# Kernel optimization log

Hardware: AMD Instinct MI355X
Metric: run time of the kernel (lower is better)

Reference implementation:

```python
import jax, jax.numpy as jnp
import numpy as np

B, Q, K, DQ, DK, H, DV = 4, 1024, 1024, 256, 256, 64, 256

def setup_inputs() -> dict:
    key = jax.random.key(0)
    k1, k2, k3, k4, k5, k6 = jax.random.split(key, 6)
    queries = jax.random.normal(k1, (B, Q, DQ), dtype=jnp.float32)
    keys = jax.random.normal(k2, (B, K, DK), dtype=jnp.float32)
    values = jax.random.normal(k3, (B, K, DV), dtype=jnp.float32)
    # learned params (stored as (in, out) so x @ W matches nn.Linear)
    W_q = jax.random.normal(k4, (DQ, H), dtype=jnp.float32) / np.sqrt(DQ)
    W_k = jax.random.normal(k5, (DK, H), dtype=jnp.float32) / np.sqrt(DK)
    w_v = jax.random.normal(k6, (H,), dtype=jnp.float32) / np.sqrt(H)
    return {"queries": queries, "keys": keys, "values": values,
            "W_q": W_q, "W_k": W_k, "w_v": w_v}

def reference(queries, keys, values, W_q, W_k, w_v):
    # projections: [B,Q,H], [B,K,H]
    q = jnp.einsum('bqd,dh->bqh', queries, W_q)
    k = jnp.einsum('bkd,dh->bkh', keys, W_k)
    # broadcast add -> tanh -> reduce with w_v: scores [B,Q,K]
    features = jnp.tanh(q[:, :, None, :] + k[:, None, :, :])  # [B,Q,K,H]
    scores = jnp.einsum('bqkh,h->bqk', features, w_v)
    attn = jax.nn.softmax(scores, axis=-1)  # dropout is identity in eval
    return jnp.einsum('bqk,bkv->bqv', attn, values)
```

## Files before the change

### kernel.cpp

```cpp
#include <hip/hip_runtime.h>

#define Bn 4
#define Qn 1024
#define Kn 1024
#define Dd 256
#define Hh 64
#define Dv 256
#define TQ 16

typedef __attribute__((ext_vector_type(8))) short short8;
typedef __attribute__((ext_vector_type(8))) _Float16 half8;
typedef __attribute__((ext_vector_type(4))) float floatx4;
typedef __attribute__((ext_vector_type(2))) float floatx2;

__device__ __forceinline__ floatx2 fma2(floatx2 a, floatx2 b, floatx2 c) {
    return __builtin_elementwise_fma(a, b, c);
}
__device__ __forceinline__ floatx2 mk2(float x, float y) {
    floatx2 r; r.x = x; r.y = y; return r;
}

__device__ __forceinline__ short f32_to_bf16(float x) {
    unsigned u = __float_as_uint(x);
    unsigned r = u + 0x7fffu + ((u >> 16) & 1u);
    return (short)(r >> 16);
}
__device__ __forceinline__ float bf16_to_f32(short h) {
    return __uint_as_float(((unsigned)(unsigned short)h) << 16);
}

__global__ __launch_bounds__(256) void prep_kernel(const float* __restrict__ Xq,
                                                   const float* __restrict__ Wq,
                                                   const float* __restrict__ Xk,
                                                   const float* __restrict__ Wk,
                                                   const float* __restrict__ V,
                                                   float* __restrict__ Eq,
                                                   float* __restrict__ Ekt,
                                                   _Float16* __restrict__ Vh) {
    int t = threadIdx.x;
    int wave = t >> 6, l = t & 63;
    if (blockIdx.x < 512) {
        int side = blockIdx.x >> 8;
        int r0 = (blockIdx.x & 255) * 16;
        int ct = wave;
        const float* X = side ? Xk : Xq;
        const float* W = side ? Wk : Wq;
        const float* xrow = X + (size_t)(r0 + (l & 15)) * Dd + (l >> 4) * 8;
        const float* wcol = W + (size_t)((l >> 4) * 8) * Hh + ct * 16 + (l & 15);

        floatx4 sxa[2], sxb[2];
        float swr[2][8];
#define PLOAD(kt, s) do {                                                   \
            sxa[s] = *(const floatx4*)(xrow + (kt) * 32);                   \
            sxb[s] = *(const floatx4*)(xrow + (kt) * 32 + 4);               \
            _Pragma("unroll")                                               \
            for (int j = 0; j < 8; ++j)                                     \
                swr[s][j] = wcol[(size_t)((kt) * 32 + j) * Hh];             \
        } while (0)

        PLOAD(0, 0);
        floatx4 acc = {0.f, 0.f, 0.f, 0.f};
        #pragma unroll
        for (int kt = 0; kt < 8; ++kt) {
            int cur = kt & 1;
            if (kt < 7) PLOAD(kt + 1, 1 - cur);
            short8 ah, al, wh, wl;
            #pragma unroll
            for (int j = 0; j < 4; ++j) {
                short hs = f32_to_bf16(sxa[cur][j]);
                ah[j] = hs;
                al[j] = f32_to_bf16(sxa[cur][j] - bf16_to_f32(hs));
                short hs2 = f32_to_bf16(sxb[cur][j]);
                ah[j + 4] = hs2;
                al[j + 4] = f32_to_bf16(sxb[cur][j] - bf16_to_f32(hs2));
            }
            #pragma unroll
            for (int j = 0; j < 8; ++j) {
                short hs = f32_to_bf16(swr[cur][j]);
                wh[j] = hs;
                wl[j] = f32_to_bf16(swr[cur][j] - bf16_to_f32(hs));
            }
            acc = __builtin_amdgcn_mfma_f32_16x16x32_bf16(ah, wh, acc, 0, 0, 0);
            acc = __builtin_amdgcn_mfma_f32_16x16x32_bf16(al, wh, acc, 0, 0, 0);
            acc = __builtin_amdgcn_mfma_f32_16x16x32_bf16(ah, wl, acc, 0, 0, 0);
        }
#undef PLOAD
        int h = ct * 16 + (l & 15);
        float e0 = __expf(2.f * acc[0]);
        float e1 = __expf(2.f * acc[1]);
        float e2 = __expf(2.f * acc[2]);
        float e3 = __expf(2.f * acc[3]);
        int row0g = r0 + (l >> 4) * 4;
        if (!side) {
            Eq[(size_t)(row0g + 0) * Hh + h] = e0;
            Eq[(size_t)(row0g + 1) * Hh + h] = e1;
            Eq[(size_t)(row0g + 2) * Hh + h] = e2;
            Eq[(size_t)(row0g + 3) * Hh + h] = e3;
        } else {
            int b = row0g >> 10, k0 = row0g & 1023;
            float4 o = { e0, e1, e2, e3 };
            *(float4*)(Ekt + ((size_t)(b * Hh + h)) * Kn + k0) = o;
        }
    } else {
        int vblk = blockIdx.x - 512;
        int b = vblk >> 5;
        int kt = vblk & 31;
        const float* Vg = V + ((size_t)(b * Kn + kt * 32 + (l >> 4) * 8)) * Dv + (l & 15);
        #pragma unroll
        for (int p = 0; p < 4; ++p) {
            int nt = wave * 4 + p;
            const float* vp = Vg + nt * 16;
            half8 hv;
            #pragma unroll
            for (int j = 0; j < 8; ++j)
                hv[j] = (_Float16)vp[(size_t)j * Dv];
            size_t base = (((size_t)(b * 32 + kt) * 16 + nt) * 512) + (size_t)l * 8;
            *(half8*)(Vh + base) = hv;
        }
    }
}

__global__ __launch_bounds__(1024, 4) void attn_kernel(const float* __restrict__ Eq,
                                                       const float* __restrict__ Ekt,
                                                       const _Float16* __restrict__ Vh,
                                                       const float* __restrict__ wv,
                                                       float* __restrict__ out) {
    __shared__ __align__(16) unsigned sc[TQ * 1028];
    __shared__ __align__(16) float qlds[TQ * Hh];
    __shared__ float wsum[16 * TQ];

    int tid = threadIdx.x;
    int blk = blockIdx.x;
    int b = (blk & 7) >> 1;
    int tile = (blk >> 3) * 2 + (blk & 1);
    int qbase = tile * TQ;

    const float* qp = Eq + (size_t)(b * Qn + qbase) * Hh;
    qlds[tid] = qp[tid];
    __syncthreads();

    const float* kb = Ekt + (size_t)b * Hh * Kn;
    const float4* wv4 = (const float4*)wv;
    floatx2 s2[TQ / 2];
    #pragma unroll
    for (int i = 0; i < TQ / 2; ++i) { s2[i].x = 0.f; s2[i].y = 0.f; }

    float e0 = kb[0 * Kn + tid];
    float e1 = kb[1 * Kn + tid];
    float e2 = kb[2 * Kn + tid];
    float e3 = kb[3 * Kn + tid];
    floatx2 one2 = mk2(1.f, 1.f);
    for (int h4 = 0; h4 < Hh / 4; ++h4) {
        float n0, n1, n2, n3;
        if (h4 < Hh / 4 - 1) {
            const float* kn = kb + (h4 + 1) * 4 * Kn;
            n0 = kn[0 * Kn + tid];
            n1 = kn[1 * Kn + tid];
            n2 = kn[2 * Kn + tid];
            n3 = kn[3 * Kn + tid];
        }
        float4 w4 = wv4[h4];
        floatx2 e0s = mk2(e0, e0), e1s = mk2(e1, e1);
        floatx2 e2s = mk2(e2, e2), e3s = mk2(e3, e3);
        floatx2 wx = mk2(w4.x, w4.x), wy = mk2(w4.y, w4.y);
        floatx2 wz = mk2(w4.z, w4.z), ww = mk2(w4.w, w4.w);
        #pragma unroll
        for (int qq = 0; qq < TQ; qq += 2) {
            float4 qva = *(const float4*)(&qlds[qq * Hh + h4 * 4]);
            float4 qvb = *(const float4*)(&qlds[(qq + 1) * Hh + h4 * 4]);
            floatx2 A = fma2(mk2(qva.x, qvb.x), e0s, one2);
            floatx2 B = fma2(mk2(qva.y, qvb.y), e1s, one2);
            floatx2 C = fma2(mk2(qva.z, qvb.z), e2s, one2);
            floatx2 D = fma2(mk2(qva.w, qvb.w), e3s, one2);
            floatx2 AB = A * B;
            floatx2 CD = C * D;
            floatx2 ABCD = AB * CD;
            floatx2 NAB = fma2(wx, B, wy * A);
            floatx2 NCD = fma2(wz, D, ww * C);
            floatx2 NUM = fma2(NCD, AB, NAB * CD);
            floatx2 R = mk2(__builtin_amdgcn_rcpf(ABCD.x),
                            __builtin_amdgcn_rcpf(ABCD.y));
            s2[qq >> 1] = fma2(NUM, R, s2[qq >> 1]);
        }
        e0 = n0; e1 = n1; e2 = n2; e3 = n3;
    }

    int wave = tid >> 6, lane = tid & 63;
    size_t vb0 = (((size_t)(b * 32) * 16 + wave) * 512) + (size_t)lane * 8;
    half8 vcur = *(const half8*)(Vh + vb0);

    _Float16* sp = (_Float16*)sc;
    float part[TQ];
    #pragma unroll
    for (int q = 0; q < TQ; ++q) {
        float sq = (q & 1) ? s2[q >> 1].y : s2[q >> 1].x;
        float p = __expf(-2.f * sq);
        part[q] = p;
        _Float16 hs = (_Float16)p;
        sp[q * 2056 + tid] = hs;
        sp[q * 2056 + 1024 + tid] = (_Float16)(p - (float)hs);
    }

    #pragma unroll
    for (int q = 0; q < TQ; ++q) {
        #pragma unroll
        for (int off = 32; off >= 1; off >>= 1)
            part[q] += __shfl_xor(part[q], off, 64);
    }
    if (lane == 0) {
        #pragma unroll
        for (int q = 0; q < TQ; ++q) wsum[wave * TQ + q] = part[q];
    }
    __syncthreads();

    int qf = lane & 15, kc = lane >> 4;
    floatx4 acc = {0.f, 0.f, 0.f, 0.f};
    const char* scb = (const char*)sc + qf * 4112 + kc * 16;
    #pragma unroll 2
    for (int kt = 0; kt < 31; ++kt) {
        half8 vnext = *(const half8*)(Vh + vb0 + (size_t)(kt + 1) * 8192);
        half8 bhi = *(const half8*)(scb + kt * 64);
        half8 blo = *(const half8*)(scb + 2048 + kt * 64);
        acc = __builtin_amdgcn_mfma_f32_16x16x32_f16(vcur, bhi, acc, 0, 0, 0);
        acc = __builtin_amdgcn_mfma_f32_16x16x32_f16(vcur, blo, acc, 0, 0, 0);
        vcur = vnext;
    }
    {
        half8 bhi = *(const half8*)(scb + 31 * 64);
        half8 blo = *(const half8*)(scb + 2048 + 31 * 64);
        acc = __builtin_amdgcn_mfma_f32_16x16x32_f16(vcur, bhi, acc, 0, 0, 0);
        acc = __builtin_amdgcn_mfma_f32_16x16x32_f16(vcur, blo, acc, 0, 0, 0);
    }
    {
        float vsum = 0.f;
        #pragma unroll
        for (int w = 0; w < 16; ++w) vsum += wsum[w * TQ + qf];
        float r = 1.f / vsum;
        float* ob = out + ((size_t)(b * Qn + qbase + qf)) * Dv + wave * 16 + kc * 4;
        float4 o = { acc[0] * r, acc[1] * r, acc[2] * r, acc[3] * r };
        *(float4*)ob = o;
    }
}

extern "C" void kernel_launch(void* const* d_in, const int* in_sizes, int n_in,
                              void* d_out, int out_size, void* d_ws, size_t ws_size,
                              hipStream_t stream) {
    const float* queries = (const float*)d_in[0];
    const float* keys    = (const float*)d_in[1];
    const float* values  = (const float*)d_in[2];
    const float* W_q     = (const float*)d_in[3];
    const float* W_k     = (const float*)d_in[4];
    const float* w_v     = (const float*)d_in[5];
    float* out = (float*)d_out;

    float* Eq  = (float*)d_ws;
    float* Ekt = Eq + Bn * Qn * Hh;
    _Float16* Vh = (_Float16*)(Ekt + Bn * Kn * Hh);

    prep_kernel<<<640, 256, 0, stream>>>(queries, W_q, keys, W_k, values,
                                         Eq, Ekt, Vh);
    attn_kernel<<<Bn * (Qn / TQ), 1024, 0, stream>>>(Eq, Ekt, Vh, w_v, out);
}
```

Measured before the change: 115.2 us.

## Fuse prep and attention into one cooperative kernel with grid sync

Merges the projection/exp prep kernel and the attention kernel into a single cooperative launch of 256 blocks. Ten waves per block do the prep jobs, then a grid-wide barrier and scalar cache invalidate separate that phase from attention. Eq is now stored transposed, so the attention phase reads q values directly from global memory as 16-wide vectors instead of staging them in LDS. This removes one kernel launch and the gap between kernels, at the cost of a grid sync, less parallelism during the prep phase, and redundant global q loads in every thread.

```diff
diff --git a/kernel.cpp b/kernel.cpp
--- a/kernel.cpp
+++ b/kernel.cpp
@@ -1,4 +1,7 @@
 #include <hip/hip_runtime.h>
+#include <hip/hip_cooperative_groups.h>
+
+namespace cg = cooperative_groups;
 
 #define Bn 4
 #define Qn 1024
@@ -12,6 +15,7 @@
 typedef __attribute__((ext_vector_type(8))) _Float16 half8;
 typedef __attribute__((ext_vector_type(4))) float floatx4;
 typedef __attribute__((ext_vector_type(2))) float floatx2;
+typedef __attribute__((ext_vector_type(16))) float floatx16;
 
 __device__ __forceinline__ floatx2 fma2(floatx2 a, floatx2 b, floatx2 c) {
     return __builtin_elementwise_fma(a, b, c);
@@ -29,105 +33,103 @@
     return __uint_as_float(((unsigned)(unsigned short)h) << 16);
 }
 
-__global__ __launch_bounds__(256) void prep_kernel(const float* __restrict__ Xq,
-                                                   const float* __restrict__ Wq,
-                                                   const float* __restrict__ Xk,
-                                                   const float* __restrict__ Wk,
-                                                   const float* __restrict__ V,
-                                                   float* __restrict__ Eq,
-                                                   float* __restrict__ Ekt,
-                                                   _Float16* __restrict__ Vh) {
-    int t = threadIdx.x;
-    int wave = t >> 6, l = t & 63;
-    if (blockIdx.x < 512) {
-        int side = blockIdx.x >> 8;
-        int r0 = (blockIdx.x & 255) * 16;
-        int ct = wave;
-        const float* X = side ? Xk : Xq;
-        const float* W = side ? Wk : Wq;
-        const float* xrow = X + (size_t)(r0 + (l & 15)) * Dd + (l >> 4) * 8;
-        const float* wcol = W + (size_t)((l >> 4) * 8) * Hh + ct * 16 + (l & 15);
-
-        floatx4 sxa[2], sxb[2];
-        float swr[2][8];
+__global__ __launch_bounds__(1024) void fused_kernel(const float* __restrict__ Xq,
+                                                     const float* __restrict__ Wq,
+                                                     const float* __restrict__ Xk,
+                                                     const float* __restrict__ Wk,
+                                                     const float* __restrict__ V,
+                                                     const float* __restrict__ wv,
+                                                     float* __restrict__ Eqt,
+                                                     float* __restrict__ Ekt,
+                                                     _Float16* __restrict__ Vh,
+                                                     float* __restrict__ out) {
+    __shared__ __align__(16) unsigned sc[TQ * 1028];
+    __shared__ float wsum[16 * TQ];
+
+    {
+        int wave = threadIdx.x >> 6, l = threadIdx.x & 63;
+        int job = blockIdx.x * 10 + wave;
+        if (wave < 10) {
+            if (job < 2048) {
+                int bo = job >> 2;
+                int side = bo >> 8;
+                int r0 = (bo & 255) * 16;
+                int ct = job & 3;
+                const float* X = side ? Xk : Xq;
+                const float* W = side ? Wk : Wq;
+                const float* xrow = X + (size_t)(r0 + (l & 15)) * Dd + (l >> 4) * 8;
+                const float* wcol = W + (size_t)((l >> 4) * 8) * Hh + ct * 16 + (l & 15);
+
+                floatx4 sxa[2], sxb[2];
+                float swr[2][8];
 #define PLOAD(kt, s) do {                                                   \
-            sxa[s] = *(const floatx4*)(xrow + (kt) * 32);                   \
-            sxb[s] = *(const floatx4*)(xrow + (kt) * 32 + 4);               \
-            _Pragma("unroll")                                               \
-            for (int j = 0; j < 8; ++j)                                     \
-                swr[s][j] = wcol[(size_t)((kt) * 32 + j) * Hh];             \
-        } while (0)
-
-        PLOAD(0, 0);
-        floatx4 acc = {0.f, 0.f, 0.f, 0.f};
-        #pragma unroll
-        for (int kt = 0; kt < 8; ++kt) {
-            int cur = kt & 1;
-            if (kt < 7) PLOAD(kt + 1, 1 - cur);
-            short8 ah, al, wh, wl;
-            #pragma unroll
-            for (int j = 0; j < 4; ++j) {
-                short hs = f32_to_bf16(sxa[cur][j]);
-                ah[j] = hs;
-                al[j] = f32_to_bf16(sxa[cur][j] - bf16_to_f32(hs));
-                short hs2 = f32_to_bf16(sxb[cur][j]);
-                ah[j + 4] = hs2;
-                al[j + 4] = f32_to_bf16(sxb[cur][j] - bf16_to_f32(hs2));
+                    sxa[s] = *(const floatx4*)(xrow + (kt) * 32);           \
+                    sxb[s] = *(const floatx4*)(xrow + (kt) * 32 + 4);       \
+                    _Pragma("unroll")                                       \
+                    for (int j = 0; j < 8; ++j)                             \
+                        swr[s][j] = wcol[(size_t)((kt) * 32 + j) * Hh];     \
+                } while (0)
+
+                PLOAD(0, 0);
+                floatx4 acc = {0.f, 0.f, 0.f, 0.f};
+                #pragma unroll
+                for (int kt = 0; kt < 8; ++kt) {
+                    int cur = kt & 1;
+                    if (kt < 7) PLOAD(kt + 1, 1 - cur);
+                    short8 ah, al, wh, wl;
+                    #pragma unroll
+                    for (int j = 0; j < 4; ++j) {
+                        short hs = f32_to_bf16(sxa[cur][j]);
+                        ah[j] = hs;
+                        al[j] = f32_to_bf16(sxa[cur][j] - bf16_to_f32(hs));
+                        short hs2 = f32_to_bf16(sxb[cur][j]);
+                        ah[j + 4] = hs2;
+                        al[j + 4] = f32_to_bf16(sxb[cur][j] - bf16_to_f32(hs2));
+                    }
+                    #pragma unroll
+                    for (int j = 0; j < 8; ++j) {
+                        short hs = f32_to_bf16(swr[cur][j]);
+                        wh[j] = hs;
+                        wl[j] = f32_to_bf16(swr[cur][j] - bf16_to_f32(hs));
+                    }
+                    acc = __builtin_amdgcn_mfma_f32_16x16x32_bf16(ah, wh, acc, 0, 0, 0);
+                    acc = __builtin_amdgcn_mfma_f32_16x16x32_bf16(al, wh, acc, 0, 0, 0);
+                    acc = __builtin_amdgcn_mfma_f32_16x16x32_bf16(ah, wl, acc, 0, 0, 0);
+                }
+#undef PLOAD
+                int h = ct * 16 + (l & 15);
+                float e0 = __expf(2.f * acc[0]);
+                float e1 = __expf(2.f * acc[1]);
+                float e2 = __expf(2.f * acc[2]);
+                float e3 = __expf(2.f * acc[3]);
+                int row0g = r0 + (l >> 4) * 4;
+                int bb = row0g >> 10, k0 = row0g & 1023;
+                float* Edst = side ? Ekt : Eqt;
+                float4 o = { e0, e1, e2, e3 };
+                *(float4*)(Edst + ((size_t)(bb * Hh + h)) * Kn + k0) = o;
+            } else {
+                int vjob = job - 2048;
+                int vblk = vjob >> 2;
+                int wv_ = vjob & 3;
+                int bb = vblk >> 5, kt = vblk & 31;
+                const float* Vg = V + ((size_t)(bb * Kn + kt * 32 + (l >> 4) * 8)) * Dv + (l & 15);
+                #pragma unroll
+                for (int p = 0; p < 4; ++p) {
+                    int nt = wv_ * 4 + p;
+                    const float* vp = Vg + nt * 16;
+                    half8 hv;
+                    #pragma unroll
+                    for (int j = 0; j < 8; ++j)
+                        hv[j] = (_Float16)vp[(size_t)j * Dv];
+                    size_t base = (((size_t)(bb * 32 + kt) * 16 + nt) * 512) + (size_t)l * 8;
+                    *(half8*)(Vh + base) = hv;
+                }
             }
-            #pragma unroll
-            for (int j = 0; j < 8; ++j) {
-                short hs = f32_to_bf16(swr[cur][j]);
-                wh[j] = hs;
-                wl[j] = f32_to_bf16(swr[cur][j] - bf16_to_f32(hs));
-            }
-            acc = __builtin_amdgcn_mfma_f32_16x16x32_bf16(ah, wh, acc, 0, 0, 0);
-            acc = __builtin_amdgcn_mfma_f32_16x16x32_bf16(al, wh, acc, 0, 0, 0);
-            acc = __builtin_amdgcn_mfma_f32_16x16x32_bf16(ah, wl, acc, 0, 0, 0);
         }
-#undef PLOAD
-        int h = ct * 16 + (l & 15);
-        float e0 = __expf(2.f * acc[0]);
-        float e1 = __expf(2.f * acc[1]);
-        float e2 = __expf(2.f * acc[2]);
-        float e3 = __expf(2.f * acc[3]);
-        int row0g = r0 + (l >> 4) * 4;
-        if (!side) {
-            Eq[(size_t)(row0g + 0) * Hh + h] = e0;
-            Eq[(size_t)(row0g + 1) * Hh + h] = e1;
-            Eq[(size_t)(row0g + 2) * Hh + h] = e2;
-            Eq[(size_t)(row0g + 3) * Hh + h] = e3;
-        } else {
-            int b = row0g >> 10, k0 = row0g & 1023;
-            float4 o = { e0, e1, e2, e3 };
-            *(float4*)(Ekt + ((size_t)(b * Hh + h)) * Kn + k0) = o;
-        }
-    } else {
-        int vblk = blockIdx.x - 512;
-        int b = vblk >> 5;
-        int kt = vblk & 31;
-        const float* Vg = V + ((size_t)(b * Kn + kt * 32 + (l >> 4) * 8)) * Dv + (l & 15);
-        #pragma unroll
-        for (int p = 0; p < 4; ++p) {
-            int nt = wave * 4 + p;
-            const float* vp = Vg + nt * 16;
-            half8 hv;
-            #pragma unroll
-            for (int j = 0; j < 8; ++j)
-                hv[j] = (_Float16)vp[(size_t)j * Dv];
-            size_t base = (((size_t)(b * 32 + kt) * 16 + nt) * 512) + (size_t)l * 8;
-            *(half8*)(Vh + base) = hv;
-        }
-    }
-}
-
-__global__ __launch_bounds__(1024, 4) void attn_kernel(const float* __restrict__ Eq,
-                                                       const float* __restrict__ Ekt,
-                                                       const _Float16* __restrict__ Vh,
-                                                       const float* __restrict__ wv,
-                                                       float* __restrict__ out) {
-    __shared__ __align__(16) unsigned sc[TQ * 1028];
-    __shared__ __align__(16) float qlds[TQ * Hh];
-    __shared__ float wsum[16 * TQ];
+    }
+
+    cg::this_grid().sync();
+    asm volatile("s_dcache_inv" ::: "memory");
 
     int tid = threadIdx.x;
     int blk = blockIdx.x;
@@ -135,11 +137,8 @@
     int tile = (blk >> 3) * 2 + (blk & 1);
     int qbase = tile * TQ;
 
-    const float* qp = Eq + (size_t)(b * Qn + qbase) * Hh;
-    qlds[tid] = qp[tid];
-    __syncthreads();
-
     const float* kb = Ekt + (size_t)b * Hh * Kn;
+    const float* qt = Eqt + (size_t)b * Hh * Qn + qbase;
     const float4* wv4 = (const float4*)wv;
     floatx2 s2[TQ / 2];
     #pragma unroll
@@ -160,18 +159,20 @@
             n3 = kn[3 * Kn + tid];
         }
         float4 w4 = wv4[h4];
+        floatx16 q0 = *(const floatx16*)(qt + (size_t)(h4 * 4 + 0) * Qn);
+        floatx16 q1 = *(const floatx16*)(qt + (size_t)(h4 * 4 + 1) * Qn);
+        floatx16 q2 = *(const floatx16*)(qt + (size_t)(h4 * 4 + 2) * Qn);
+        floatx16 q3 = *(const floatx16*)(qt + (size_t)(h4 * 4 + 3) * Qn);
         floatx2 e0s = mk2(e0, e0), e1s = mk2(e1, e1);
         floatx2 e2s = mk2(e2, e2), e3s = mk2(e3, e3);
         floatx2 wx = mk2(w4.x, w4.x), wy = mk2(w4.y, w4.y);
         floatx2 wz = mk2(w4.z, w4.z), ww = mk2(w4.w, w4.w);
         #pragma unroll
         for (int qq = 0; qq < TQ; qq += 2) {
-            float4 qva = *(const float4*)(&qlds[qq * Hh + h4 * 4]);
-            float4 qvb = *(const float4*)(&qlds[(qq + 1) * Hh + h4 * 4]);
-            floatx2 A = fma2(mk2(qva.x, qvb.x), e0s, one2);
-            floatx2 B = fma2(mk2(qva.y, qvb.y), e1s, one2);
-            floatx2 C = fma2(mk2(qva.z, qvb.z), e2s, one2);
-            floatx2 D = fma2(mk2(qva.w, qvb.w), e3s, one2);
+            floatx2 A = fma2(mk2(q0[qq], q0[qq + 1]), e0s, one2);
+            floatx2 B = fma2(mk2(q1[qq], q1[qq + 1]), e1s, one2);
+            floatx2 C = fma2(mk2(q2[qq], q2[qq + 1]), e2s, one2);
+            floatx2 D = fma2(mk2(q3[qq], q3[qq + 1]), e3s, one2);
             floatx2 AB = A * B;
             floatx2 CD = C * D;
             floatx2 ABCD = AB * CD;
@@ -253,11 +254,13 @@
     const float* w_v     = (const float*)d_in[5];
     float* out = (float*)d_out;
 
-    float* Eq  = (float*)d_ws;
-    float* Ekt = Eq + Bn * Qn * Hh;
+    float* Eqt = (float*)d_ws;
+    float* Ekt = Eqt + Bn * Qn * Hh;
     _Float16* Vh = (_Float16*)(Ekt + Bn * Kn * Hh);
 
-    prep_kernel<<<640, 256, 0, stream>>>(queries, W_q, keys, W_k, values,
-                                         Eq, Ekt, Vh);
-    attn_kernel<<<Bn * (Qn / TQ), 1024, 0, stream>>>(Eq, Ekt, Vh, w_v, out);
-}
+    void* args[] = { (void*)&queries, (void*)&W_q, (void*)&keys, (void*)&W_k,
+                     (void*)&values,  (void*)&w_v, (void*)&Eqt,  (void*)&Ekt,
+                     (void*)&Vh, (void*)&out };
+    hipLaunchCooperativeKernel((const void*)fused_kernel, dim3(256), dim3(1024),
+                               args, 0, stream);
+}
```

Measured after the change: 160.8 us. 39.6% more time.
